# Kernel optimization log

Measured on AMD Instinct MI355X. Metric: run time of the kernel, lower is better.

Reference implementation:

```python
import jax, jax.numpy as jnp
import numpy as np

B = 128          # number of graphs in the batch
NM, EM = 100000, 400000    # mol nodes / edges
NP, EP = 200000, 3200000   # protein nodes / edges
DM, DP, OD = 78, 54, 16


def setup_inputs() -> dict:
    key = jax.random.key(0)
    ks = jax.random.split(key, 20)
    def w(k, shape):
        return jax.random.normal(k, shape, jnp.float32) * 0.05
    z = lambda n: jnp.zeros((n,), jnp.float32)
    return {
        "mol_x": jax.random.normal(ks[0], (NM, DM), jnp.float32),
        "mol_edge_index": jax.random.randint(ks[1], (2, EM), 0, NM),
        "mol_batch": jnp.sort(jax.random.randint(ks[2], (NM,), 0, B)),
        "pro_x": jax.random.normal(ks[3], (NP, DP), jnp.float32),
        "pro_edge_index": jax.random.randint(ks[4], (2, EP), 0, NP),
        "pro_batch": jnp.sort(jax.random.randint(ks[5], (NP,), 0, B)),
        "mol_W1": w(ks[6], (256, DM)), "mol_b1": z(256),
        "mol_W2": w(ks[7], (7 * OD, 256)), "mol_b2": z(7 * OD),
        "c1_Wl": w(ks[8], (DP, DP)), "c1_bl": z(DP), "c1_Wr": w(ks[9], (DP, DP)),
        "c2_Wl": w(ks[10], (2 * DP, DP)), "c2_bl": z(2 * DP), "c2_Wr": w(ks[11], (2 * DP, DP)),
        "pro_W1": w(ks[12], (256, 2 * DP)), "pro_b1": z(256),
        "pro_W2": w(ks[13], (9 * OD, 256)), "pro_b2": z(9 * OD),
        "fc1_W": w(ks[14], (1024, 16 * OD)), "fc1_b": z(1024),
        "fc2_W": w(ks[15], (512, 1024)), "fc2_b": z(512),
        "out_W": w(ks[16], (1, 512)), "out_b": z(1),
    }


def _seg_mean(x, seg, n):
    s = jax.ops.segment_sum(x, seg, num_segments=n)
    c = jax.ops.segment_sum(jnp.ones((x.shape[0],), x.dtype), seg, num_segments=n)
    return s / jnp.maximum(c, 1.0)[:, None]


def _sage(x, ei, Wl, bl, Wr):
    # PyG SAGEConv (mean aggr): lin_l(mean_{j->i} x_j) + lin_r(x_i); lin_r has no bias
    agg = _seg_mean(x[ei[0]], ei[1], x.shape[0])
    return agg @ Wl.T + bl + x @ Wr.T


def reference(mol_x, mol_edge_index, mol_batch, pro_x, pro_edge_index, pro_batch,
              mol_W1, mol_b1, mol_W2, mol_b2,
              c1_Wl, c1_bl, c1_Wr, c2_Wl, c2_bl, c2_Wr,
              pro_W1, pro_b1, pro_W2, pro_b2,
              fc1_W, fc1_b, fc2_W, fc2_b, out_W, out_b):
    alpha, degree = 0.05, 4
    # APPNP-style k-hop propagation over the unnormalized COO adjacency:
    # (adj @ h)[i] = sum over edges (row=i, col=j) of h[j]
    row, col = mol_edge_index[0], mol_edge_index[1]
    h = mol_x
    emb = alpha * mol_x
    for _ in range(degree):
        h = jax.ops.segment_sum(h[col], row, num_segments=mol_x.shape[0])
        emb = emb + (1.0 - alpha) * h / degree
    x = _seg_mean(emb, mol_batch, B)            # global mean pool -> [B, 78]
    x = jax.nn.relu(x @ mol_W1.T + mol_b1)
    x = x @ mol_W2.T + mol_b2                   # [B, 112]; dropout is identity at eval

    xt = jax.nn.relu(_sage(pro_x, pro_edge_index, c1_Wl, c1_bl, c1_Wr))
    xt = jax.nn.relu(_sage(xt, pro_edge_index, c2_Wl, c2_bl, c2_Wr))
    xt = _seg_mean(xt, pro_batch, B)            # [B, 108]
    xt = jax.nn.relu(xt @ pro_W1.T + pro_b1)
    xt = xt @ pro_W2.T + pro_b2                 # [B, 144]

    xc = jnp.concatenate([x, xt], axis=1)       # [B, 256]
    xc = jax.nn.relu(xc @ fc1_W.T + fc1_b)
    xc = jax.nn.relu(xc @ fc2_W.T + fc2_b)
    return xc @ out_W.T + out_b                 # [B, 1]
```

## Files before the change

### kernel.cpp

```cpp
#include <hip/hip_runtime.h>

#define K256 __launch_bounds__(256)

constexpr int B = 128;
constexpr int NM = 100000, EM = 400000;
constexpr int NP = 200000, EP = 3200000;
constexpr int DM = 78, DPK = 54, DP2 = 108;
constexpr int XH = 32;

__device__ __forceinline__ float b2f(unsigned short u) {
  return __uint_as_float((unsigned int)u << 16);
}
__device__ __forceinline__ unsigned short f2b(float f) {
  unsigned int b = __float_as_uint(f);
  return (unsigned short)((b + 0x7fffu + ((b >> 16) & 1u)) >> 16);
}

template <int SH>
__global__ void K256 k_bhist(const int* __restrict__ dst, int* __restrict__ bhist, int E) {
  __shared__ int lh[512];
  int tid = threadIdx.x;
  for (int t = tid; t < 512; t += 256) lh[t] = 0;
  __syncthreads();
  int c0 = blockIdx.x * 4096;
#pragma unroll
  for (int k = 0; k < 16; k++) {
    int e = c0 + k * 256 + tid;
    if (e < E) atomicAdd(&lh[dst[e] >> SH], 1);
  }
  __syncthreads();
  for (int t = tid; t < 512; t += 256) {
    int c = lh[t];
    if (c) atomicAdd(&bhist[t], c);
  }
}

__global__ void k_scanb(const int* __restrict__ bhist, int* __restrict__ bed,
                        int* __restrict__ bcur, int NB, int E) {
  __shared__ int s[512];
  int tid = threadIdx.x;
  int v = (tid < NB) ? bhist[tid] : 0;
  s[tid] = v;
  __syncthreads();
  for (int off = 1; off < 512; off <<= 1) {
    int t = (tid >= off) ? s[tid - off] : 0;
    __syncthreads();
    s[tid] += t;
    __syncthreads();
  }
  int excl = s[tid] - v;
  if (tid < NB) {
    bed[tid] = excl;
    bcur[tid] = excl;
  }
  if (tid == NB - 1) bed[NB] = E;
}

template <int SH>
__global__ void K256 k_bin(const int* __restrict__ src, const int* __restrict__ dst,
                           int* __restrict__ bcur, int2* __restrict__ binned, int E) {
  __shared__ int lh[512];
  __shared__ int gbase[512];
  int c0 = blockIdx.x * 4096;
  int tid = threadIdx.x;
  for (int t = tid; t < 512; t += 256) lh[t] = 0;
  __syncthreads();
  int r[16], dcache[16];
#pragma unroll
  for (int k = 0; k < 16; k++) {
    int e = c0 + k * 256 + tid;
    if (e < E) {
      int d = dst[e];
      dcache[k] = d;
      r[k] = atomicAdd(&lh[d >> SH], 1);
    }
  }
  __syncthreads();
  for (int b = tid; b < 512; b += 256) {
    int c = lh[b];
    gbase[b] = c ? atomicAdd(&bcur[b], c) : 0;
  }
  __syncthreads();
#pragma unroll
  for (int k = 0; k < 16; k++) {
    int e = c0 + k * 256 + tid;
    if (e < E) {
      int d = dcache[k];
      binned[gbase[d >> SH] + r[k]] = make_int2(src[e], d);
    }
  }
}

template <int SH>
__global__ void K256 k_build(const int2* __restrict__ binned, const int* __restrict__ bed,
                             int* __restrict__ deg, int* __restrict__ starts,
                             int* __restrict__ csr, int N) {
  constexpr int NN = 1 << SH;
  constexpr int P = NN / 256;
  __shared__ int lcnt[NN];
  __shared__ int lpair[256];
  int b = blockIdx.x, base = b << SH, tid = threadIdx.x;
  int nn = min(N - base, NN);
  for (int t = tid; t < NN; t += 256) lcnt[t] = 0;
  __syncthreads();
  int e0 = bed[b], e1 = bed[b + 1];
  for (int e = e0 + tid; e < e1; e += 256) atomicAdd(&lcnt[binned[e].y - base], 1);
  __syncthreads();
  int loc[P];
  int psum = 0;
#pragma unroll
  for (int p = 0; p < P; p++) {
    loc[p] = lcnt[tid * P + p];
    psum += loc[p];
  }
  lpair[tid] = psum;
  __syncthreads();
  for (int off = 1; off < 256; off <<= 1) {
    int t = (tid >= off) ? lpair[tid - off] : 0;
    __syncthreads();
    lpair[tid] += t;
    __syncthreads();
  }
  int run = lpair[tid] - psum;
  __syncthreads();
#pragma unroll
  for (int p = 0; p < P; p++) {
    int i = tid * P + p;
    int st = e0 + run;
    if (i < nn) {
      deg[base + i] = loc[p];
      starts[base + i] = st;
    }
    lcnt[i] = st;
    run += loc[p];
  }
  __syncthreads();
  for (int e = e0 + tid; e < e1; e += 256) {
    int2 sd = binned[e];
    int p = atomicAdd(&lcnt[sd.y - base], 1);
    csr[p] = sd.x;
  }
}

__global__ void K256 k_bstart(const int* __restrict__ batch, int* __restrict__ bstart, int N) {
  int i = blockIdx.x * 256 + threadIdx.x;
  if (i < N) {
    int b = batch[i];
    int pb = (i == 0) ? -1 : batch[i - 1];
    for (int bb = pb + 1; bb <= b; bb++) bstart[bb] = i;
    if (i == N - 1)
      for (int bb = b + 1; bb <= B; bb++) bstart[bb] = N;
  }
}

__global__ void k_inv(const int* __restrict__ bstart, float* __restrict__ inv) {
  int b = threadIdx.x;
  if (b < B) inv[b] = 1.f / fmaxf((float)(bstart[b + 1] - bstart[b]), 1.f);
}

__global__ void K256 k_transT(const float* __restrict__ in, float* __restrict__ out, int R,
                              int C) {
  __shared__ float t[32][33];
  int cb = blockIdx.x * 32, rb = blockIdx.y * 32;
  int tx = threadIdx.x & 31, ty = threadIdx.x >> 5;
  for (int i = ty; i < 32; i += 8) {
    int r = rb + i, c = cb + tx;
    if (r < R && c < C) t[i][tx] = in[(size_t)r * C + c];
  }
  __syncthreads();
  for (int i = ty; i < 32; i += 8) {
    int c = cb + i, r = rb + tx;
    if (r < R && c < C) out[(size_t)c * R + r] = t[tx][i];
  }
}

__global__ void K256 k_prepw(const float* __restrict__ c1Wl, const float* __restrict__ c1Wr,
                             const float* __restrict__ c1bl, const float* __restrict__ c2Wl,
                             const float* __restrict__ c2Wr, float* __restrict__ w1cat,
                             float* __restrict__ bl1c, float* __restrict__ w2cat) {
  int i = blockIdx.x * 256 + threadIdx.x;
  if (i < 108 * 56) {
    int k = i / 56, o = i - k * 56;
    w1cat[i] = (o < 54) ? ((k < 54) ? c1Wl[o * 54 + k] : c1Wr[o * 54 + (k - 54)]) : 0.f;
  }
  if (i < 108 * 108) {
    int k = i / 108, o = i - k * 108;
    w2cat[i] = (k < 54) ? c2Wl[o * 54 + k] : c2Wr[o * 54 + (k - 54)];
  }
  if (i < 56) bl1c[i] = (i < 54) ? c1bl[i] : 0.f;
}

__global__ void K256 k_cast(const float* __restrict__ x, ushort2* __restrict__ xh, int N) {
  int t = blockIdx.x * 256 + threadIdx.x;
  if (t < N * 27) {
    int n = t / 27, j = t - n * 27;
    float2 v = *(const float2*)(x + (size_t)n * 54 + 2 * j);
    xh[(size_t)n * XH + j] = make_ushort2(f2b(v.x), f2b(v.y));
  }
}

__global__ void K256 k_gatherh(const ushort2* __restrict__ xh, const int* __restrict__ starts,
                               const int* __restrict__ deg, const int* __restrict__ csr,
                               ushort2* __restrict__ outh, int N) {
  int wid = (blockIdx.x * 256 + threadIdx.x) >> 6;
  int lane = threadIdx.x & 63;
  if (wid >= N) return;
  int s = starts[wid], d = deg[wid];
  const int* cp = csr + s;
  int half = lane >> 5, sl = lane & 31;
  bool act = sl < 27;
  float ax = 0.f, ay = 0.f, bx = 0.f, by = 0.f;
  float cx = 0.f, cy = 0.f, dx = 0.f, dy = 0.f;
  int j = 0;
  for (; j + 8 <= d; j += 8) {
    if (act) {
      ushort2 v0 = xh[(size_t)cp[j + half] * XH + sl];
      ushort2 v1 = xh[(size_t)cp[j + 2 + half] * XH + sl];
      ushort2 v2 = xh[(size_t)cp[j + 4 + half] * XH + sl];
      ushort2 v3 = xh[(size_t)cp[j + 6 + half] * XH + sl];
      ax += b2f(v0.x);
      ay += b2f(v0.y);
      bx += b2f(v1.x);
      by += b2f(v1.y);
      cx += b2f(v2.x);
      cy += b2f(v2.y);
      dx += b2f(v3.x);
      dy += b2f(v3.y);
    }
  }
  for (; j + 2 <= d; j += 2) {
    if (act) {
      ushort2 v = xh[(size_t)cp[j + half] * XH + sl];
      ax += b2f(v.x);
      ay += b2f(v.y);
    }
  }
  if (j < d && half == 0 && act) {
    ushort2 v = xh[(size_t)cp[j] * XH + sl];
    ax += b2f(v.x);
    ay += b2f(v.y);
  }
  ax += bx + cx + dx;
  ay += by + cy + dy;
  ax += __shfl_xor(ax, 32, 64);
  ay += __shfl_xor(ay, 32, 64);
  if (half == 0 && act) {
    float inv = 1.f / fmaxf((float)d, 1.f);
    outh[(size_t)wid * XH + sl] = make_ushort2(f2b(ax * inv), f2b(ay * inv));
  }
}

template <int D, bool MEAN>
__global__ void K256 k_gatherv(const float* __restrict__ x, const int* __restrict__ starts,
                               const int* __restrict__ deg, const int* __restrict__ csr,
                               float* __restrict__ out, int N, int ostride) {
  constexpr int NF2 = D / 2;
  int wid = (blockIdx.x * 256 + threadIdx.x) >> 6;
  int lane = threadIdx.x & 63;
  if (wid >= N) return;
  int s = starts[wid], d = deg[wid];
  const int* cp = csr + s;
  bool act = lane < NF2;
  float ax = 0.f, ay = 0.f, bx = 0.f, by = 0.f;
  int j = 0;
  for (; j + 4 <= d; j += 4) {
    if (act) {
      float2 v0 = ((const float2*)(x + (size_t)cp[j] * D))[lane];
      float2 v1 = ((const float2*)(x + (size_t)cp[j + 1] * D))[lane];
      float2 v2 = ((const float2*)(x + (size_t)cp[j + 2] * D))[lane];
      float2 v3 = ((const float2*)(x + (size_t)cp[j + 3] * D))[lane];
      ax += v0.x + v2.x;
      ay += v0.y + v2.y;
      bx += v1.x + v3.x;
      by += v1.y + v3.y;
    }
  }
  for (; j < d; j++) {
    if (act) {
      float2 v = ((const float2*)(x + (size_t)cp[j] * D))[lane];
      ax += v.x;
      ay += v.y;
    }
  }
  ax += bx;
  ay += by;
  if (act) {
    float inv = MEAN ? 1.f / fmaxf((float)d, 1.f) : 1.f;
    float2* op = (float2*)(out + (size_t)wid * ostride);
    float2 w;
    w.x = ax * inv;
    w.y = ay * inv;
    op[lane] = w;
  }
}

template <int D, int SPLIT>
__global__ void K256 k_pool_seg2(const float* __restrict__ x, const int* __restrict__ bstart,
                                 float* __restrict__ pooled, float coef) {
  constexpr int NPB = 256 / D;
  __shared__ float sp[D * NPB];
  int b = blockIdx.x / SPLIT;
  int sidx = blockIdx.x - b * SPLIT;
  int tid = threadIdx.x;
  int r0 = bstart[b], r1 = bstart[b + 1];
  int len = r1 - r0;
  int per = (len + SPLIT - 1) / SPLIT;
  int s0 = r0 + sidx * per;
  int s1 = min(r1, s0 + per);
  if (tid < D * NPB) {
    int ioff = tid / D, f = tid - ioff * D;
    float a0 = 0.f, a1 = 0.f, a2 = 0.f, a3 = 0.f;
    int i = s0 + ioff;
    for (; i + 3 * NPB < s1; i += 4 * NPB) {
      a0 += x[(size_t)i * D + f];
      a1 += x[(size_t)(i + NPB) * D + f];
      a2 += x[(size_t)(i + 2 * NPB) * D + f];
      a3 += x[(size_t)(i + 3 * NPB) * D + f];
    }
    for (; i < s1; i += NPB) a0 += x[(size_t)i * D + f];
    sp[tid] = (a0 + a1) + (a2 + a3);
  }
  __syncthreads();
  if (tid < D) {
    float s = 0.f;
#pragma unroll
    for (int g = 0; g < NPB; g++) s += sp[g * D + tid];
    s *= coef;
    if (s != 0.f) atomicAdd(&pooled[b * D + tid], s);
  }
}

__global__ void __launch_bounds__(256, 4) k_sage1c(
    const float* __restrict__ x, const ushort2* __restrict__ aggh,
    const float* __restrict__ wcat, const float* __restrict__ blc,
    ushort2* __restrict__ outh, int N) {
  __shared__ float scat[64 * 109];
  int base = blockIdx.x * 64;
  int nn = min(N - base, 64);
  int tid = threadIdx.x;
  for (int t = tid; t < nn * 27; t += 256) {
    int n = t / 27, j = t - n * 27;
    ushort2 va = aggh[(size_t)(base + n) * XH + j];
    float2 vx = *(const float2*)(x + (size_t)(base + n) * 54 + 2 * j);
    float* sr = scat + n * 109;
    sr[2 * j] = b2f(va.x);
    sr[2 * j + 1] = b2f(va.y);
    sr[54 + 2 * j] = vx.x;
    sr[54 + 2 * j + 1] = vx.y;
  }
  __syncthreads();
  int w = tid >> 6, lane = tid & 63;
  int obase = __builtin_amdgcn_readfirstlane(w * 14);
  if (lane >= nn) return;
  float acc[14];
#pragma unroll
  for (int o = 0; o < 14; o++) acc[o] = blc[obase + o];
  const float* rs = scat + lane * 109;
#pragma unroll 2
  for (int k = 0; k < 108; k++) {
    float v = rs[k];
    const float* wr = wcat + k * 56 + obase;
#pragma unroll
    for (int o = 0; o < 14; o++) acc[o] += v * wr[o];
  }
  ushort2* op = outh + (size_t)(base + lane) * XH + (obase >> 1);
#pragma unroll
  for (int o = 0; o < 7; o++)
    op[o] = make_ushort2(f2b(fmaxf(acc[2 * o], 0.f)), f2b(fmaxf(acc[2 * o + 1], 0.f)));
}

template <int SPLIT>
__global__ void __launch_bounds__(256, 4) k_sage2c(
    const ushort2* __restrict__ xt1h, const ushort2* __restrict__ aggh,
    const float* __restrict__ wcat, const float* __restrict__ bl,
    const int* __restrict__ bstart, float* __restrict__ pooled) {
  __shared__ float scat[64 * 109];
  int b = blockIdx.x / SPLIT;
  int sidx = blockIdx.x - b * SPLIT;
  int tid = threadIdx.x;
  int w = tid >> 6, lane = tid & 63;
  int obase = __builtin_amdgcn_readfirstlane(w * 27);
  int r0 = bstart[b], r1 = bstart[b + 1];
  int len = r1 - r0;
  int per = (len + SPLIT - 1) / SPLIT;
  int s0 = r0 + sidx * per;
  int s1 = min(r1, s0 + per);
  float pool[27];
#pragma unroll
  for (int o = 0; o < 27; o++) pool[o] = 0.f;
  for (int tb = s0; tb < s1; tb += 64) {
    int nn = min(s1 - tb, 64);
    __syncthreads();
    for (int t = tid; t < nn * 27; t += 256) {
      int n = t / 27, j = t - n * 27;
      ushort2 va = aggh[(size_t)(tb + n) * XH + j];
      ushort2 vx = xt1h[(size_t)(tb + n) * XH + j];
      float* sr = scat + n * 109;
      sr[2 * j] = b2f(va.x);
      sr[2 * j + 1] = b2f(va.y);
      sr[54 + 2 * j] = b2f(vx.x);
      sr[54 + 2 * j + 1] = b2f(vx.y);
    }
    __syncthreads();
    if (lane < nn) {
      float acc[27];
#pragma unroll
      for (int o = 0; o < 27; o++) acc[o] = bl[obase + o];
      const float* rs = scat + lane * 109;
#pragma unroll 2
      for (int k = 0; k < 108; k++) {
        float v = rs[k];
        const float* wr = wcat + k * 108 + obase;
#pragma unroll
        for (int o = 0; o < 27; o++) acc[o] += v * wr[o];
      }
#pragma unroll
      for (int o = 0; o < 27; o++) pool[o] += fmaxf(acc[o], 0.f);
    }
  }
#pragma unroll
  for (int o = 0; o < 27; o++) {
#pragma unroll
    for (int off = 1; off < 64; off <<= 1) pool[o] += __shfl_xor(pool[o], off, 64);
  }
  if (lane == 0) {
    float* pb = pooled + b * DP2 + obase;
#pragma unroll
    for (int o = 0; o < 27; o++)
      if (pool[o] != 0.f) atomicAdd(&pb[o], pool[o]);
  }
}

template <int DIN, int DOUT, bool RELU>
__global__ void K256 k_mlp(const float* __restrict__ X, int xstride,
                           const float* __restrict__ rs, const float* __restrict__ WT,
                           const float* __restrict__ bias, float* __restrict__ Y,
                           int ystride, int ycol0) {
  constexpr int BT = 8;
  __shared__ float Xs[BT][DIN];
  int tid = threadIdx.x;
  int ob = blockIdx.x * 256 + tid;
  int bb = blockIdx.y * BT;
  for (int t = tid; t < BT * DIN; t += 256) {
    int i = t / DIN, k = t - i * DIN;
    float v = X[(size_t)(bb + i) * xstride + k];
    if (rs) v *= rs[bb + i];
    Xs[i][k] = v;
  }
  __syncthreads();
  int o = (ob < DOUT) ? ob : (DOUT - 1);
  float bv = bias[o];
  float acc[BT];
#pragma unroll
  for (int i = 0; i < BT; i++) acc[i] = bv;
#pragma unroll 4
  for (int k = 0; k < DIN; k++) {
    float w = WT[(size_t)k * DOUT + o];
#pragma unroll
    for (int i = 0; i < BT; i++) acc[i] += Xs[i][k] * w;
  }
  if (ob < DOUT) {
#pragma unroll
    for (int i = 0; i < BT; i++) {
      float v = RELU ? fmaxf(acc[i], 0.f) : acc[i];
      Y[(size_t)(bb + i) * ystride + ycol0 + ob] = v;
    }
  }
}

__global__ void __launch_bounds__(64) k_gemv1(const float* __restrict__ t2,
                                              const float* __restrict__ W3,
                                              const float* __restrict__ b3,
                                              float* __restrict__ out) {
  int b = blockIdx.x, lane = threadIdx.x;
  float a = 0.f;
  const float* row = t2 + (size_t)b * 512;
#pragma unroll 2
  for (int k = lane; k < 512; k += 64) a += row[k] * W3[k];
#pragma unroll
  for (int off = 32; off > 0; off >>= 1) a += __shfl_down(a, off, 64);
  if (lane == 0) out[b] = a + b3[0];
}

__global__ void k_report(float* out, float v, int n) {
  int i = blockIdx.x * 256 + threadIdx.x;
  if (i < n) out[i] = v;
}

extern "C" void kernel_launch(void* const* d_in, const int* in_sizes, int n_in,
                              void* d_out, int out_size, void* d_ws, size_t ws_size,
                              hipStream_t stream) {
  (void)in_sizes; (void)n_in;
  const float* mol_x = (const float*)d_in[0];
  const int* m_ei = (const int*)d_in[1];
  const int* m_batch = (const int*)d_in[2];
  const float* pro_x = (const float*)d_in[3];
  const int* p_ei = (const int*)d_in[4];
  const int* p_batch = (const int*)d_in[5];
  const float* mol_W1 = (const float*)d_in[6];
  const float* mol_b1 = (const float*)d_in[7];
  const float* mol_W2 = (const float*)d_in[8];
  const float* mol_b2 = (const float*)d_in[9];
  const float* c1_Wl = (const float*)d_in[10];
  const float* c1_bl = (const float*)d_in[11];
  const float* c1_Wr = (const float*)d_in[12];
  const float* c2_Wl = (const float*)d_in[13];
  const float* c2_bl = (const float*)d_in[14];
  const float* c2_Wr = (const float*)d_in[15];
  const float* pro_W1 = (const float*)d_in[16];
  const float* pro_b1 = (const float*)d_in[17];
  const float* pro_W2 = (const float*)d_in[18];
  const float* pro_b2 = (const float*)d_in[19];
  const float* fc1_W = (const float*)d_in[20];
  const float* fc1_b = (const float*)d_in[21];
  const float* fc2_W = (const float*)d_in[22];
  const float* fc2_b = (const float*)d_in[23];
  const float* out_W = (const float*)d_in[24];
  const float* out_b = (const float*)d_in[25];
  float* out = (float*)d_out;
  char* ws = (char*)d_ws;

  const int* m_row = m_ei;
  const int* m_col = m_ei + EM;
  const int* p_e0 = p_ei;
  const int* p_e1 = p_ei + EP;

  auto al = [](size_t x) { return (x + 255) & ~(size_t)255; };

  size_t o = 0;
  size_t o_pdeg = o;   o += al((size_t)NP * 4);
  size_t o_pstart = o; o += al((size_t)NP * 4);
  size_t o_pcsr = o;   o += al((size_t)EP * 4);
  size_t o_aggh = o;   o += al((size_t)NP * XH * 4);
  size_t o_xt1h = o;   o += al((size_t)NP * XH * 4);
  size_t o_pxh = o;    o += al((size_t)NP * XH * 4);
  size_t pro_end = o;

  o = 0;
  size_t o_mdeg = o;   o += al((size_t)NM * 4);
  size_t o_mstart = o; o += al((size_t)NM * 4);
  size_t o_mcsr = o;   o += al((size_t)EM * 4);
  size_t o_hA = o;     o += al((size_t)NM * DM * 4);
  size_t o_hB = o;     o += al((size_t)NM * DM * 4);
  size_t mol_end = o;

  size_t tail = al(pro_end > mol_end ? pro_end : mol_end);
  size_t o_poolM = tail; tail += al((size_t)B * DM * 4);
  size_t o_poolP = tail; tail += al((size_t)B * DP2 * 4);
  size_t o_mbs = tail;   tail += al((size_t)(B + 1) * 4);
  size_t o_pbs = tail;   tail += al((size_t)(B + 1) * 4);
  size_t o_w1c = tail;   tail += al((size_t)108 * 56 * 4);
  size_t o_bl1 = tail;   tail += al(56 * 4);
  size_t o_w2c = tail;   tail += al((size_t)108 * 108 * 4);
  size_t o_mbc = tail;   tail += al(512 * 4);
  size_t o_pbc = tail;   tail += al(512 * 4);
  size_t o_mbh = tail;   tail += al(512 * 4);
  size_t o_pbh = tail;   tail += al(512 * 4);
  size_t o_mbed = tail;  tail += al(513 * 4);
  size_t o_pbed = tail;  tail += al(513 * 4);
  size_t o_mh1T = tail;  tail += al((size_t)DM * 256 * 4);
  size_t o_mh2T = tail;  tail += al((size_t)256 * 112 * 4);
  size_t o_ph1T = tail;  tail += al((size_t)DP2 * 256 * 4);
  size_t o_ph2T = tail;  tail += al((size_t)256 * 144 * 4);
  size_t o_fc1T = tail;  tail += al((size_t)256 * 1024 * 4);
  size_t o_fc2T = tail;  tail += al((size_t)1024 * 512 * 4);
  size_t o_xc = tail;    tail += al((size_t)B * 256 * 4);
  size_t o_t1 = tail;    tail += al((size_t)B * 1024 * 4);
  size_t o_t2 = tail;    tail += al((size_t)B * 512 * 4);
  size_t o_th = tail;    tail += al((size_t)B * 256 * 4);
  size_t o_invM = tail;  tail += al(B * 4);
  size_t o_invP = tail;  tail += al(B * 4);

  if (ws_size < tail) {
    k_report<<<1, 256, 0, stream>>>(out, (float)(ws_size >> 20), out_size);
    return;
  }

  int* mdeg = (int*)(ws + o_mdeg);
  int* mstart = (int*)(ws + o_mstart);
  int* mcsr = (int*)(ws + o_mcsr);
  float* hA = (float*)(ws + o_hA);
  float* hB = (float*)(ws + o_hB);
  int* pdeg = (int*)(ws + o_pdeg);
  int* pstart = (int*)(ws + o_pstart);
  int* pcsr = (int*)(ws + o_pcsr);
  ushort2* aggh = (ushort2*)(ws + o_aggh);
  ushort2* xt1h = (ushort2*)(ws + o_xt1h);
  ushort2* pxh = (ushort2*)(ws + o_pxh);
  float* poolM = (float*)(ws + o_poolM);
  float* poolP = (float*)(ws + o_poolP);
  int* mbs = (int*)(ws + o_mbs);
  int* pbs = (int*)(ws + o_pbs);
  float* w1cat = (float*)(ws + o_w1c);
  float* bl1c = (float*)(ws + o_bl1);
  float* w2cat = (float*)(ws + o_w2c);
  int* mbc = (int*)(ws + o_mbc);
  int* pbc = (int*)(ws + o_pbc);
  int* mbh = (int*)(ws + o_mbh);
  int* pbh = (int*)(ws + o_pbh);
  int* mbed = (int*)(ws + o_mbed);
  int* pbed = (int*)(ws + o_pbed);
  float* mh1T = (float*)(ws + o_mh1T);
  float* mh2T = (float*)(ws + o_mh2T);
  float* ph1T = (float*)(ws + o_ph1T);
  float* ph2T = (float*)(ws + o_ph2T);
  float* fc1T = (float*)(ws + o_fc1T);
  float* fc2T = (float*)(ws + o_fc2T);
  float* xc = (float*)(ws + o_xc);
  float* t1 = (float*)(ws + o_t1);
  float* t2 = (float*)(ws + o_t2);
  float* th = (float*)(ws + o_th);
  float* invM = (float*)(ws + o_invM);
  float* invP = (float*)(ws + o_invP);
  int2* mbinned = (int2*)hA;
  int2* pbinned = (int2*)aggh;

  k_prepw<<<(108 * 108 + 255) / 256, 256, 0, stream>>>(c1_Wl, c1_Wr, c1_bl, c2_Wl, c2_Wr,
                                                       w1cat, bl1c, w2cat);
  {
    auto tg = [](int R, int C) { return dim3((C + 31) / 32, (R + 31) / 32); };
    k_transT<<<tg(256, DM), 256, 0, stream>>>(mol_W1, mh1T, 256, DM);
    k_transT<<<tg(112, 256), 256, 0, stream>>>(mol_W2, mh2T, 112, 256);
    k_transT<<<tg(256, DP2), 256, 0, stream>>>(pro_W1, ph1T, 256, DP2);
    k_transT<<<tg(144, 256), 256, 0, stream>>>(pro_W2, ph2T, 144, 256);
    k_transT<<<tg(1024, 256), 256, 0, stream>>>(fc1_W, fc1T, 1024, 256);
    k_transT<<<tg(512, 1024), 256, 0, stream>>>(fc2_W, fc2T, 512, 1024);
  }

  constexpr int SHM = 8;
  constexpr int NBM = (NM + (1 << SHM) - 1) >> SHM;
  hipMemsetAsync(mbh, 0, 512 * 4, stream);
  hipMemsetAsync(poolM, 0, (size_t)B * DM * 4, stream);
  k_bhist<SHM><<<(EM + 4095) / 4096, 256, 0, stream>>>(m_row, mbh, EM);
  k_scanb<<<1, 512, 0, stream>>>(mbh, mbed, mbc, NBM, EM);
  k_bin<SHM><<<(EM + 4095) / 4096, 256, 0, stream>>>(m_col, m_row, mbc, mbinned, EM);
  k_build<SHM><<<NBM, 256, 0, stream>>>(mbinned, mbed, mdeg, mstart, mcsr, NM);
  k_bstart<<<(NM + 255) / 256, 256, 0, stream>>>(m_batch, mbs, NM);
  k_inv<<<1, 128, 0, stream>>>(mbs, invM);

  int gb_m = (NM * 64 + 255) / 256;
  k_pool_seg2<DM, 8><<<B * 8, 256, 0, stream>>>(mol_x, mbs, poolM, 0.05f);
  k_gatherv<DM, false><<<gb_m, 256, 0, stream>>>(mol_x, mstart, mdeg, mcsr, hA, NM, DM);
  k_pool_seg2<DM, 8><<<B * 8, 256, 0, stream>>>(hA, mbs, poolM, 0.2375f);
  k_gatherv<DM, false><<<gb_m, 256, 0, stream>>>(hA, mstart, mdeg, mcsr, hB, NM, DM);
  k_pool_seg2<DM, 8><<<B * 8, 256, 0, stream>>>(hB, mbs, poolM, 0.2375f);
  k_gatherv<DM, false><<<gb_m, 256, 0, stream>>>(hB, mstart, mdeg, mcsr, hA, NM, DM);
  k_pool_seg2<DM, 8><<<B * 8, 256, 0, stream>>>(hA, mbs, poolM, 0.2375f);
  k_gatherv<DM, false><<<gb_m, 256, 0, stream>>>(hA, mstart, mdeg, mcsr, hB, NM, DM);
  k_pool_seg2<DM, 8><<<B * 8, 256, 0, stream>>>(hB, mbs, poolM, 0.2375f);
  {
    dim3 g1(1, B / 8);
    k_mlp<DM, 256, true><<<g1, 256, 0, stream>>>(poolM, DM, invM, mh1T, mol_b1, th, 256, 0);
    k_mlp<256, 112, false><<<g1, 256, 0, stream>>>(th, 256, nullptr, mh2T, mol_b2, xc, 256, 0);
  }

  constexpr int SHP = 9;
  constexpr int NBP = (NP + (1 << SHP) - 1) >> SHP;
  hipMemsetAsync(pbh, 0, 512 * 4, stream);
  hipMemsetAsync(poolP, 0, (size_t)B * DP2 * 4, stream);
  k_bhist<SHP><<<(EP + 4095) / 4096, 256, 0, stream>>>(p_e1, pbh, EP);
  k_scanb<<<1, 512, 0, stream>>>(pbh, pbed, pbc, NBP, EP);
  k_bin<SHP><<<(EP + 4095) / 4096, 256, 0, stream>>>(p_e0, p_e1, pbc, pbinned, EP);
  k_build<SHP><<<NBP, 256, 0, stream>>>(pbinned, pbed, pdeg, pstart, pcsr, NP);
  k_bstart<<<(NP + 255) / 256, 256, 0, stream>>>(p_batch, pbs, NP);
  k_inv<<<1, 128, 0, stream>>>(pbs, invP);
  k_cast<<<(NP * 27 + 255) / 256, 256, 0, stream>>>(pro_x, pxh, NP);

  int gb_p = (NP * 64 + 255) / 256;
  k_gatherh<<<gb_p, 256, 0, stream>>>(pxh, pstart, pdeg, pcsr, aggh, NP);
  k_sage1c<<<(NP + 63) / 64, 256, 0, stream>>>(pro_x, aggh, w1cat, bl1c, xt1h, NP);
  k_gatherh<<<gb_p, 256, 0, stream>>>(xt1h, pstart, pdeg, pcsr, aggh, NP);
  k_sage2c<8><<<B * 8, 256, 0, stream>>>(xt1h, aggh, w2cat, c2_bl, pbs, poolP);
  {
    dim3 g1(1, B / 8);
    k_mlp<DP2, 256, true><<<g1, 256, 0, stream>>>(poolP, DP2, invP, ph1T, pro_b1, th, 256, 0);
    k_mlp<256, 144, false><<<g1, 256, 0, stream>>>(th, 256, nullptr, ph2T, pro_b2, xc, 256, 112);
  }

  {
    dim3 gA(4, B / 8);
    k_mlp<256, 1024, true><<<gA, 256, 0, stream>>>(xc, 256, nullptr, fc1T, fc1_b, t1, 1024, 0);
    dim3 gB(2, B / 8);
    k_mlp<1024, 512, true><<<gB, 256, 0, stream>>>(t1, 1024, nullptr, fc2T, fc2_b, t2, 512, 0);
    k_gemv1<<<B, 64, 0, stream>>>(t2, out_W, out_b, out);
  }
}
```

Measured before the change: 903.6 us.

## Store molecule propagation in bf16 and widen protein gather to 8-byte loads

The molecule APPNP propagation now casts mol_x to bf16 in a padded 48-pair layout, and the gathers and pooling run on bf16 intermediates instead of fp32. This halves the bytes moved per hop. The protein SAGE gather now loads ushort4 with four neighbors per wave in flight and reduces with two shuffles, giving wider memory transactions. The cost is bf16 rounding of unnormalized sums over four hops, which could hurt accuracy as magnitudes grow.

```diff
diff --git a/kernel.cpp b/kernel.cpp
--- a/kernel.cpp
+++ b/kernel.cpp
@@ -7,6 +7,8 @@
 constexpr int NP = 200000, EP = 3200000;
 constexpr int DM = 78, DPK = 54, DP2 = 108;
 constexpr int XH = 32;
+constexpr int XH4 = 16;
+constexpr int MH = 48;
 
 __device__ __forceinline__ float b2f(unsigned short u) {
   return __uint_as_float((unsigned int)u << 16);
@@ -190,16 +192,81 @@
   if (i < 56) bl1c[i] = (i < 54) ? c1bl[i] : 0.f;
 }
 
-__global__ void K256 k_cast(const float* __restrict__ x, ushort2* __restrict__ xh, int N) {
+template <int DF2, int XHD>
+__global__ void K256 k_castg(const float* __restrict__ x, int sstride,
+                             ushort2* __restrict__ xh, int N) {
   int t = blockIdx.x * 256 + threadIdx.x;
-  if (t < N * 27) {
-    int n = t / 27, j = t - n * 27;
-    float2 v = *(const float2*)(x + (size_t)n * 54 + 2 * j);
-    xh[(size_t)n * XH + j] = make_ushort2(f2b(v.x), f2b(v.y));
-  }
-}
-
-__global__ void K256 k_gatherh(const ushort2* __restrict__ xh, const int* __restrict__ starts,
+  if (t < N * DF2) {
+    int n = t / DF2, j = t - n * DF2;
+    float2 v = *(const float2*)(x + (size_t)n * sstride + 2 * j);
+    xh[(size_t)n * XHD + j] = make_ushort2(f2b(v.x), f2b(v.y));
+  }
+}
+
+__global__ void K256 k_gatherh(const ushort4* __restrict__ xh4, const int* __restrict__ starts,
+                               const int* __restrict__ deg, const int* __restrict__ csr,
+                               ushort4* __restrict__ outh4, int N) {
+  int wid = (blockIdx.x * 256 + threadIdx.x) >> 6;
+  int lane = threadIdx.x & 63;
+  if (wid >= N) return;
+  int s = starts[wid], d = deg[wid];
+  const int* cp = csr + s;
+  int quarter = lane >> 4, sl = lane & 15;
+  bool act = sl < 14;
+  float a0 = 0.f, a1 = 0.f, a2 = 0.f, a3 = 0.f;
+  float b0 = 0.f, b1 = 0.f, b2 = 0.f, b3 = 0.f;
+  int j = 0;
+  for (; j + 8 <= d; j += 8) {
+    if (act) {
+      ushort4 v = xh4[(size_t)cp[j + quarter] * XH4 + sl];
+      ushort4 w = xh4[(size_t)cp[j + 4 + quarter] * XH4 + sl];
+      a0 += b2f(v.x);
+      a1 += b2f(v.y);
+      a2 += b2f(v.z);
+      a3 += b2f(v.w);
+      b0 += b2f(w.x);
+      b1 += b2f(w.y);
+      b2 += b2f(w.z);
+      b3 += b2f(w.w);
+    }
+  }
+  for (; j + 4 <= d; j += 4) {
+    if (act) {
+      ushort4 v = xh4[(size_t)cp[j + quarter] * XH4 + sl];
+      a0 += b2f(v.x);
+      a1 += b2f(v.y);
+      a2 += b2f(v.z);
+      a3 += b2f(v.w);
+    }
+  }
+  int r = d - j;
+  if (quarter < r && act) {
+    ushort4 v = xh4[(size_t)cp[j + quarter] * XH4 + sl];
+    a0 += b2f(v.x);
+    a1 += b2f(v.y);
+    a2 += b2f(v.z);
+    a3 += b2f(v.w);
+  }
+  a0 += b0;
+  a1 += b1;
+  a2 += b2;
+  a3 += b3;
+  a0 += __shfl_xor(a0, 16, 64);
+  a1 += __shfl_xor(a1, 16, 64);
+  a2 += __shfl_xor(a2, 16, 64);
+  a3 += __shfl_xor(a3, 16, 64);
+  a0 += __shfl_xor(a0, 32, 64);
+  a1 += __shfl_xor(a1, 32, 64);
+  a2 += __shfl_xor(a2, 32, 64);
+  a3 += __shfl_xor(a3, 32, 64);
+  if (lane < 14) {
+    float inv = 1.f / fmaxf((float)d, 1.f);
+    outh4[(size_t)wid * XH4 + lane] =
+        make_ushort4(f2b(a0 * inv), f2b(a1 * inv), f2b(a2 * inv), f2b(a3 * inv));
+  }
+}
+
+__global__ void K256 k_gatherm(const ushort2* __restrict__ xh, const int* __restrict__ starts,
                                const int* __restrict__ deg, const int* __restrict__ csr,
                                ushort2* __restrict__ outh, int N) {
   int wid = (blockIdx.x * 256 + threadIdx.x) >> 6;
@@ -207,98 +274,38 @@
   if (wid >= N) return;
   int s = starts[wid], d = deg[wid];
   const int* cp = csr + s;
-  int half = lane >> 5, sl = lane & 31;
-  bool act = sl < 27;
-  float ax = 0.f, ay = 0.f, bx = 0.f, by = 0.f;
-  float cx = 0.f, cy = 0.f, dx = 0.f, dy = 0.f;
-  int j = 0;
-  for (; j + 8 <= d; j += 8) {
-    if (act) {
-      ushort2 v0 = xh[(size_t)cp[j + half] * XH + sl];
-      ushort2 v1 = xh[(size_t)cp[j + 2 + half] * XH + sl];
-      ushort2 v2 = xh[(size_t)cp[j + 4 + half] * XH + sl];
-      ushort2 v3 = xh[(size_t)cp[j + 6 + half] * XH + sl];
-      ax += b2f(v0.x);
-      ay += b2f(v0.y);
-      bx += b2f(v1.x);
-      by += b2f(v1.y);
-      cx += b2f(v2.x);
-      cy += b2f(v2.y);
-      dx += b2f(v3.x);
-      dy += b2f(v3.y);
-    }
-  }
-  for (; j + 2 <= d; j += 2) {
-    if (act) {
-      ushort2 v = xh[(size_t)cp[j + half] * XH + sl];
-      ax += b2f(v.x);
-      ay += b2f(v.y);
-    }
-  }
-  if (j < d && half == 0 && act) {
-    ushort2 v = xh[(size_t)cp[j] * XH + sl];
-    ax += b2f(v.x);
-    ay += b2f(v.y);
-  }
-  ax += bx + cx + dx;
-  ay += by + cy + dy;
-  ax += __shfl_xor(ax, 32, 64);
-  ay += __shfl_xor(ay, 32, 64);
-  if (half == 0 && act) {
-    float inv = 1.f / fmaxf((float)d, 1.f);
-    outh[(size_t)wid * XH + sl] = make_ushort2(f2b(ax * inv), f2b(ay * inv));
-  }
-}
-
-template <int D, bool MEAN>
-__global__ void K256 k_gatherv(const float* __restrict__ x, const int* __restrict__ starts,
-                               const int* __restrict__ deg, const int* __restrict__ csr,
-                               float* __restrict__ out, int N, int ostride) {
-  constexpr int NF2 = D / 2;
-  int wid = (blockIdx.x * 256 + threadIdx.x) >> 6;
-  int lane = threadIdx.x & 63;
-  if (wid >= N) return;
-  int s = starts[wid], d = deg[wid];
-  const int* cp = csr + s;
-  bool act = lane < NF2;
+  bool act = lane < 39;
   float ax = 0.f, ay = 0.f, bx = 0.f, by = 0.f;
   int j = 0;
   for (; j + 4 <= d; j += 4) {
     if (act) {
-      float2 v0 = ((const float2*)(x + (size_t)cp[j] * D))[lane];
-      float2 v1 = ((const float2*)(x + (size_t)cp[j + 1] * D))[lane];
-      float2 v2 = ((const float2*)(x + (size_t)cp[j + 2] * D))[lane];
-      float2 v3 = ((const float2*)(x + (size_t)cp[j + 3] * D))[lane];
-      ax += v0.x + v2.x;
-      ay += v0.y + v2.y;
-      bx += v1.x + v3.x;
-      by += v1.y + v3.y;
+      ushort2 v0 = xh[(size_t)cp[j] * MH + lane];
+      ushort2 v1 = xh[(size_t)cp[j + 1] * MH + lane];
+      ushort2 v2 = xh[(size_t)cp[j + 2] * MH + lane];
+      ushort2 v3 = xh[(size_t)cp[j + 3] * MH + lane];
+      ax += b2f(v0.x) + b2f(v2.x);
+      ay += b2f(v0.y) + b2f(v2.y);
+      bx += b2f(v1.x) + b2f(v3.x);
+      by += b2f(v1.y) + b2f(v3.y);
     }
   }
   for (; j < d; j++) {
     if (act) {
-      float2 v = ((const float2*)(x + (size_t)cp[j] * D))[lane];
-      ax += v.x;
-      ay += v.y;
+      ushort2 v = xh[(size_t)cp[j] * MH + lane];
+      ax += b2f(v.x);
+      ay += b2f(v.y);
     }
   }
   ax += bx;
   ay += by;
-  if (act) {
-    float inv = MEAN ? 1.f / fmaxf((float)d, 1.f) : 1.f;
-    float2* op = (float2*)(out + (size_t)wid * ostride);
-    float2 w;
-    w.x = ax * inv;
-    w.y = ay * inv;
-    op[lane] = w;
-  }
-}
-
-template <int D, int SPLIT>
-__global__ void K256 k_pool_seg2(const float* __restrict__ x, const int* __restrict__ bstart,
+  if (act) outh[(size_t)wid * MH + lane] = make_ushort2(f2b(ax), f2b(ay));
+}
+
+template <int SPLIT>
+__global__ void K256 k_pool_segh(const ushort2* __restrict__ xh, const int* __restrict__ bstart,
                                  float* __restrict__ pooled, float coef) {
-  constexpr int NPB = 256 / D;
-  __shared__ float sp[D * NPB];
+  constexpr int NPB = 6;
+  __shared__ float sp[NPB * DM];
   int b = blockIdx.x / SPLIT;
   int sidx = blockIdx.x - b * SPLIT;
   int tid = threadIdx.x;
@@ -307,26 +314,35 @@
   int per = (len + SPLIT - 1) / SPLIT;
   int s0 = r0 + sidx * per;
   int s1 = min(r1, s0 + per);
-  if (tid < D * NPB) {
-    int ioff = tid / D, f = tid - ioff * D;
-    float a0 = 0.f, a1 = 0.f, a2 = 0.f, a3 = 0.f;
+  if (tid < 39 * NPB) {
+    int ioff = tid / 39, j = tid - ioff * 39;
+    float a0x = 0.f, a0y = 0.f, a1x = 0.f, a1y = 0.f;
     int i = s0 + ioff;
     for (; i + 3 * NPB < s1; i += 4 * NPB) {
-      a0 += x[(size_t)i * D + f];
-      a1 += x[(size_t)(i + NPB) * D + f];
-      a2 += x[(size_t)(i + 2 * NPB) * D + f];
-      a3 += x[(size_t)(i + 3 * NPB) * D + f];
-    }
-    for (; i < s1; i += NPB) a0 += x[(size_t)i * D + f];
-    sp[tid] = (a0 + a1) + (a2 + a3);
-  }
-  __syncthreads();
-  if (tid < D) {
+      ushort2 v0 = xh[(size_t)i * MH + j];
+      ushort2 v1 = xh[(size_t)(i + NPB) * MH + j];
+      ushort2 v2 = xh[(size_t)(i + 2 * NPB) * MH + j];
+      ushort2 v3 = xh[(size_t)(i + 3 * NPB) * MH + j];
+      a0x += b2f(v0.x) + b2f(v2.x);
+      a0y += b2f(v0.y) + b2f(v2.y);
+      a1x += b2f(v1.x) + b2f(v3.x);
+      a1y += b2f(v1.y) + b2f(v3.y);
+    }
+    for (; i < s1; i += NPB) {
+      ushort2 v = xh[(size_t)i * MH + j];
+      a0x += b2f(v.x);
+      a0y += b2f(v.y);
+    }
+    sp[ioff * DM + 2 * j] = a0x + a1x;
+    sp[ioff * DM + 2 * j + 1] = a0y + a1y;
+  }
+  __syncthreads();
+  if (tid < DM) {
     float s = 0.f;
 #pragma unroll
-    for (int g = 0; g < NPB; g++) s += sp[g * D + tid];
+    for (int g = 0; g < NPB; g++) s += sp[g * DM + tid];
     s *= coef;
-    if (s != 0.f) atomicAdd(&pooled[b * D + tid], s);
+    if (s != 0.f) atomicAdd(&pooled[b * DM + tid], s);
   }
 }
 
@@ -540,8 +556,9 @@
   size_t o_mdeg = o;   o += al((size_t)NM * 4);
   size_t o_mstart = o; o += al((size_t)NM * 4);
   size_t o_mcsr = o;   o += al((size_t)EM * 4);
-  size_t o_hA = o;     o += al((size_t)NM * DM * 4);
-  size_t o_hB = o;     o += al((size_t)NM * DM * 4);
+  size_t o_mxh = o;    o += al((size_t)NM * MH * 4);
+  size_t o_hAh = o;    o += al((size_t)NM * MH * 4);
+  size_t o_hBh = o;    o += al((size_t)NM * MH * 4);
   size_t mol_end = o;
 
   size_t tail = al(pro_end > mol_end ? pro_end : mol_end);
@@ -579,8 +596,9 @@
   int* mdeg = (int*)(ws + o_mdeg);
   int* mstart = (int*)(ws + o_mstart);
   int* mcsr = (int*)(ws + o_mcsr);
-  float* hA = (float*)(ws + o_hA);
-  float* hB = (float*)(ws + o_hB);
+  ushort2* mxh = (ushort2*)(ws + o_mxh);
+  ushort2* hAh = (ushort2*)(ws + o_hAh);
+  ushort2* hBh = (ushort2*)(ws + o_hBh);
   int* pdeg = (int*)(ws + o_pdeg);
   int* pstart = (int*)(ws + o_pstart);
   int* pcsr = (int*)(ws + o_pcsr);
@@ -612,7 +630,7 @@
   float* th = (float*)(ws + o_th);
   float* invM = (float*)(ws + o_invM);
   float* invP = (float*)(ws + o_invP);
-  int2* mbinned = (int2*)hA;
+  int2* mbinned = (int2*)hAh;
   int2* pbinned = (int2*)aggh;
 
   k_prepw<<<(108 * 108 + 255) / 256, 256, 0, stream>>>(c1_Wl, c1_Wr, c1_bl, c2_Wl, c2_Wr,
@@ -637,17 +655,18 @@
   k_build<SHM><<<NBM, 256, 0, stream>>>(mbinned, mbed, mdeg, mstart, mcsr, NM);
   k_bstart<<<(NM + 255) / 256, 256, 0, stream>>>(m_batch, mbs, NM);
   k_inv<<<1, 128, 0, stream>>>(mbs, invM);
+  k_castg<39, MH><<<(NM * 39 + 255) / 256, 256, 0, stream>>>(mol_x, DM, mxh, NM);
 
   int gb_m = (NM * 64 + 255) / 256;
-  k_pool_seg2<DM, 8><<<B * 8, 256, 0, stream>>>(mol_x, mbs, poolM, 0.05f);
-  k_gatherv<DM, false><<<gb_m, 256, 0, stream>>>(mol_x, mstart, mdeg, mcsr, hA, NM, DM);
-  k_pool_seg2<DM, 8><<<B * 8, 256, 0, stream>>>(hA, mbs, poolM, 0.2375f);
-  k_gatherv<DM, false><<<gb_m, 256, 0, stream>>>(hA, mstart, mdeg, mcsr, hB, NM, DM);
-  k_pool_seg2<DM, 8><<<B * 8, 256, 0, stream>>>(hB, mbs, poolM, 0.2375f);
-  k_gatherv<DM, false><<<gb_m, 256, 0, stream>>>(hB, mstart, mdeg, mcsr, hA, NM, DM);
-  k_pool_seg2<DM, 8><<<B * 8, 256, 0, stream>>>(hA, mbs, poolM, 0.2375f);
-  k_gatherv<DM, false><<<gb_m, 256, 0, stream>>>(hA, mstart, mdeg, mcsr, hB, NM, DM);
-  k_pool_seg2<DM, 8><<<B * 8, 256, 0, stream>>>(hB, mbs, poolM, 0.2375f);
+  k_pool_segh<8><<<B * 8, 256, 0, stream>>>(mxh, mbs, poolM, 0.05f);
+  k_gatherm<<<gb_m, 256, 0, stream>>>(mxh, mstart, mdeg, mcsr, hAh, NM);
+  k_pool_segh<8><<<B * 8, 256, 0, stream>>>(hAh, mbs, poolM, 0.2375f);
+  k_gatherm<<<gb_m, 256, 0, stream>>>(hAh, mstart, mdeg, mcsr, hBh, NM);
+  k_pool_segh<8><<<B * 8, 256, 0, stream>>>(hBh, mbs, poolM, 0.2375f);
+  k_gatherm<<<gb_m, 256, 0, stream>>>(hBh, mstart, mdeg, mcsr, hAh, NM);
+  k_pool_segh<8><<<B * 8, 256, 0, stream>>>(hAh, mbs, poolM, 0.2375f);
+  k_gatherm<<<gb_m, 256, 0, stream>>>(hAh, mstart, mdeg, mcsr, hBh, NM);
+  k_pool_segh<8><<<B * 8, 256, 0, stream>>>(hBh, mbs, poolM, 0.2375f);
   {
     dim3 g1(1, B / 8);
     k_mlp<DM, 256, true><<<g1, 256, 0, stream>>>(poolM, DM, invM, mh1T, mol_b1, th, 256, 0);
@@ -664,12 +683,14 @@
   k_build<SHP><<<NBP, 256, 0, stream>>>(pbinned, pbed, pdeg, pstart, pcsr, NP);
   k_bstart<<<(NP + 255) / 256, 256, 0, stream>>>(p_batch, pbs, NP);
   k_inv<<<1, 128, 0, stream>>>(pbs, invP);
-  k_cast<<<(NP * 27 + 255) / 256, 256, 0, stream>>>(pro_x, pxh, NP);
+  k_castg<27, XH><<<(NP * 27 + 255) / 256, 256, 0, stream>>>(pro_x, DPK, pxh, NP);
 
   int gb_p = (NP * 64 + 255) / 256;
-  k_gatherh<<<gb_p, 256, 0, stream>>>(pxh, pstart, pdeg, pcsr, aggh, NP);
+  k_gatherh<<<gb_p, 256, 0, stream>>>((const ushort4*)pxh, pstart, pdeg, pcsr,
+                                      (ushort4*)aggh, NP);
   k_sage1c<<<(NP + 63) / 64, 256, 0, stream>>>(pro_x, aggh, w1cat, bl1c, xt1h, NP);
-  k_gatherh<<<gb_p, 256, 0, stream>>>(xt1h, pstart, pdeg, pcsr, aggh, NP);
+  k_gatherh<<<gb_p, 256, 0, stream>>>((const ushort4*)xt1h, pstart, pdeg, pcsr,
+                                      (ushort4*)aggh, NP);
   k_sage2c<8><<<B * 8, 256, 0, stream>>>(xt1h, aggh, w2cat, c2_bl, pbs, poolP);
   {
     dim3 g1(1, B / 8);
```

New measurement: 867.1 us. -4.0%, faster.
